# Kernel tuning notes

Measured on AMD Instinct MI355X. Metric: run time of the kernel, lower is better.

The kernel has to match this reference:

```python
import jax, jax.numpy as jnp
import numpy as np

N, DIM, K = 65536, 256, 4096

def setup_inputs() -> dict:
    key = jax.random.key(0)
    kx, kc = jax.random.split(key)
    x = jax.random.normal(kx, (N, DIM), dtype=jnp.float32)
    codebook = jax.random.normal(kc, (K, DIM), dtype=jnp.float32) * 0.02
    return {"x": x, "codebook": codebook}

def reference(x, codebook):
    # torch.cdist(x, codebook).argmin(-1) == argmin of squared distances;
    x_sq = jnp.sum(x * x, axis=-1, keepdims=True)           # (n, 1)
    c_sq = jnp.sum(codebook * codebook, axis=-1)            # (k,)
    dots = jnp.einsum('nd,kd->nk', x, codebook)             # (n, k) GEMM
    dist_sq = x_sq - 2.0 * dots + c_sq[None, :]             # (n, k)
    indices = jnp.argmin(dist_sq, axis=-1)                  # (n,)
    quantized = jnp.take(codebook, indices, axis=0)         # (n, dim) gather
    return (quantized, indices)
```

## Files before the change

### kernel.cpp

```cpp
#include <hip/hip_runtime.h>
#include <cfloat>

typedef _Float16 half8 __attribute__((ext_vector_type(8)));
typedef float    f32x4 __attribute__((ext_vector_type(4)));

#define N_ROWS 65536
#define DIM    256
#define KCODES 4096
#define BM 128
#define BN 128
#define BK 32
#define NSLICE (DIM / BK)
#define NCHUNK (KCODES / BN)

#define WS_CSQ 0
#define WS_CH  278528
#define WS_CL  2375680

#define GLDS(g, l) __builtin_amdgcn_global_load_lds(                       \
    (const __attribute__((address_space(1))) unsigned int*)(g),            \
    (__attribute__((address_space(3))) unsigned int*)(l), 16, 0, 0)

__global__ void prep_codes(const float* __restrict__ cb, float* __restrict__ csq,
                           _Float16* __restrict__ ch, _Float16* __restrict__ cl) {
    __shared__ float As[32 * DIM];
    const int t = threadIdx.x;
    const int c0 = blockIdx.x * 32;
    #pragma unroll
    for (int i = 0; i < 8; ++i) {
        int r = 4 * i + (t >> 6), d4 = (t & 63) * 4;
        *(float4*)&As[r * DIM + d4] = *(const float4*)&cb[(size_t)(c0 + r) * DIM + d4];
    }
    __syncthreads();
    {
        const int r = t >> 3;
        const int k0 = (t & 7) * 32;
        const float* src = &As[r * DIM + k0];
        _Float16* dh = &ch[(size_t)(c0 + r) * DIM + k0];
        _Float16* dl = &cl[(size_t)(c0 + r) * DIM + k0];
        #pragma unroll
        for (int i = 0; i < 4; ++i) {
            half8 hv, lv;
            #pragma unroll
            for (int j = 0; j < 8; ++j) {
                float sv = src[i * 8 + j] * 64.f;
                _Float16 h = (_Float16)sv;
                hv[j] = h; lv[j] = (_Float16)(sv - (float)h);
            }
            *(half8*)(dh + i * 8) = hv;
            *(half8*)(dl + i * 8) = lv;
        }
    }
    if (t < 32) {
        const float* row = &As[t * DIM];
        float s = 0.f;
        for (int k = 0; k < DIM; ++k) s = fmaf(row[k], row[k], s);
        csq[c0 + t] = s;
    }
}

__global__ __launch_bounds__(256, 2)
void vq_mfma(const float* __restrict__ x, const float* __restrict__ cb,
             const float* __restrict__ csq,
             const _Float16* __restrict__ ch, const _Float16* __restrict__ cl,
             float* out_q, float* __restrict__ out_idx) {
    __shared__ _Float16 LDS[8 * BM * BK];
    _Float16* AhS = LDS;
    _Float16* AlS = LDS + 2 * BM * BK;
    _Float16* BhS = LDS + 4 * BM * BK;
    _Float16* BlS = LDS + 6 * BM * BK;

    const int t = threadIdx.x;
    const int lane = t & 63, wave = t >> 6;
    const int wy = wave >> 1, wx = wave & 1;
    const int m = lane & 15, q = lane >> 4;
    const int n0 = blockIdx.x * BM;
    const int swz = (q ^ ((m + (m >> 2)) & 3)) * 8;

    {
        float*  prepF = (float*)LDS;
        double* dtmp  = (double*)(LDS + 4 * BM * BK);
        float*  xsqS  = (float*)(LDS + 6 * BM * BK);
        char*   xqw   = (char*)out_q;
        for (int g = 0; g < 4; ++g) {
            const int r0 = g * 32;
            #pragma unroll
            for (int i = 0; i < 8; ++i) {
                int r = 4 * i + (t >> 6), d4 = (t & 63) * 4;
                *(float4*)&prepF[r * DIM + d4] =
                    *(const float4*)&x[(size_t)(n0 + r0 + r) * DIM + d4];
            }
            __syncthreads();
            {
                const int r = t >> 3;
                const int col8 = (t & 7) * 8;
                char* dst = xqw + (((size_t)(n0 + r0 + r)) << 10) + (size_t)(col8 * 2);
                const float* src = &prepF[r * DIM + col8];
                #pragma unroll
                for (int i = 0; i < 4; ++i) {
                    half8 hv, lv;
                    #pragma unroll
                    for (int j = 0; j < 8; ++j) {
                        float v = src[i * 64 + j];
                        _Float16 h = (_Float16)v;
                        hv[j] = h; lv[j] = (_Float16)(v - (float)h);
                    }
                    *(half8*)(dst + i * 128) = hv;
                    *(half8*)(dst + 512 + i * 128) = lv;
                }
            }
            if (t < 128) {
                int r = t >> 2, part = t & 3;
                const float* ap = &prepF[r * DIM + 64 * part];
                double s = 0.0;
                for (int k = 0; k < 64; ++k) { double v = (double)ap[k]; s = fma(v, v, s); }
                dtmp[t] = s;
            }
            __syncthreads();
            if (t < 32)
                xsqS[r0 + t] = (float)((dtmp[4*t] + dtmp[4*t+1]) + (dtmp[4*t+2] + dtmp[4*t+3]));
            __syncthreads();
        }
    }

    float xsq_r[16];
    {
        const float* xsqS = (const float*)(LDS + 6 * BM * BK);
        #pragma unroll
        for (int s = 0; s < 16; ++s)
            xsq_r[s] = xsqS[64 * wy + 16 * (s >> 2) + 4 * q + (s & 3)];
    }
    asm volatile("s_waitcnt vmcnt(0)" ::: "memory");
    __syncthreads();

    const int rq  = lane >> 2;
    const int gph = lane & 3;
    const int glogB = ((gph ^ ((rq + (rq >> 2)) & 3)) << 4);
    const char* xqb = (const char*)out_q;
    const char* aBase  = xqb + (((size_t)(n0 + wave * 32 + rq)) << 10) + glogB;
    const char* bBaseH = (const char*)ch + (((size_t)(wave * 32 + rq)) << 9) + glogB;
    const char* bBaseL = (const char*)cl + (((size_t)(wave * 32 + rq)) << 9) + glogB;

#define STAGE(ck2, sl2, nb) do {                                             \
    const char* a_  = aBase  + (size_t)((sl2) * 64);                         \
    const size_t bo_ = ((size_t)(ck2) << 16) + (size_t)((sl2) * 64);         \
    const char* bh_ = bBaseH + bo_;                                          \
    const char* bl_ = bBaseL + bo_;                                          \
    _Float16* Ah_ = AhS + (nb) * (BM * BK) + wave * (32 * BK);               \
    _Float16* Al_ = AlS + (nb) * (BM * BK) + wave * (32 * BK);               \
    _Float16* Bh_ = BhS + (nb) * (BN * BK) + wave * (32 * BK);               \
    _Float16* Bl_ = BlS + (nb) * (BN * BK) + wave * (32 * BK);               \
    GLDS(a_,           Ah_);                                                 \
    GLDS(a_ + 16384,   Ah_ + 16 * BK);                                       \
    GLDS(a_ + 512,     Al_);                                                 \
    GLDS(a_ + 16896,   Al_ + 16 * BK);                                       \
    GLDS(bh_,          Bh_);                                                 \
    GLDS(bh_ + 8192,   Bh_ + 16 * BK);                                       \
    GLDS(bl_,          Bl_);                                                 \
    GLDS(bl_ + 8192,   Bl_ + 16 * BK);                                       \
} while (0)

    int aoffs[4], boffs[4];
    #pragma unroll
    for (int tr = 0; tr < 4; ++tr) aoffs[tr] = (64 * wy + 16 * tr + m) * BK + swz;
    #pragma unroll
    for (int tc = 0; tc < 4; ++tc) boffs[tc] = (64 * wx + 16 * tc + m) * BK + swz;

    float best[16]; int bidx[16];
    #pragma unroll
    for (int s = 0; s < 16; ++s) { best[s] = FLT_MAX; bidx[s] = 0; }

    STAGE(0, 0, 0);
    STAGE(0, 1, 1);
    asm volatile("s_waitcnt vmcnt(8)" ::: "memory");
    __builtin_amdgcn_s_barrier();
    __builtin_amdgcn_sched_barrier(0);

    for (int chunk = 0; chunk < NCHUNK; ++chunk) {
        const int c0 = chunk * BN;
        float csq_c[4];
        #pragma unroll
        for (int tc = 0; tc < 4; ++tc) csq_c[tc] = csq[c0 + 64 * wx + 16 * tc + m];

        f32x4 acc[4][4];
        #pragma unroll
        for (int tr = 0; tr < 4; ++tr)
            #pragma unroll
            for (int tc = 0; tc < 4; ++tc) acc[tr][tc] = (f32x4){0.f, 0.f, 0.f, 0.f};

        #pragma unroll
        for (int sl = 0; sl < NSLICE; ++sl) {
            const int cbuf = sl & 1;
            const _Float16* Ahr = AhS + cbuf * (BM * BK);
            const _Float16* Alr = AlS + cbuf * (BM * BK);
            const _Float16* Bhr = BhS + cbuf * (BN * BK);
            const _Float16* Blr = BlS + cbuf * (BN * BK);

            half8 aH[4], aL[4], bH[4], bL[4];
            #pragma unroll
            for (int tr = 0; tr < 4; ++tr) {
                aH[tr] = *(const half8*)&Ahr[aoffs[tr]];
                aL[tr] = *(const half8*)&Alr[aoffs[tr]];
            }
            #pragma unroll
            for (int tc = 0; tc < 4; ++tc) {
                bH[tc] = *(const half8*)&Bhr[boffs[tc]];
                bL[tc] = *(const half8*)&Blr[boffs[tc]];
            }

            const int sl2r = sl + 2;
            const int ck2 = chunk + (sl2r >> 3);
            const int sl2 = sl2r & 7;
            const bool stg = (ck2 < NCHUNK);
            if (stg) {
                asm volatile("s_waitcnt lgkmcnt(0)" ::: "memory");
                __builtin_amdgcn_s_barrier();
                __builtin_amdgcn_sched_barrier(0);
                STAGE(ck2, sl2, cbuf);
            }

            #pragma unroll
            for (int tc = 0; tc < 4; ++tc)
                #pragma unroll
                for (int tr = 0; tr < 4; ++tr)
                    acc[tr][tc] = __builtin_amdgcn_mfma_f32_16x16x32_f16(aH[tr], bH[tc], acc[tr][tc], 0, 0, 0);
            #pragma unroll
            for (int tc = 0; tc < 4; ++tc)
                #pragma unroll
                for (int tr = 0; tr < 4; ++tr)
                    acc[tr][tc] = __builtin_amdgcn_mfma_f32_16x16x32_f16(aH[tr], bL[tc], acc[tr][tc], 0, 0, 0);
            #pragma unroll
            for (int tc = 0; tc < 4; ++tc)
                #pragma unroll
                for (int tr = 0; tr < 4; ++tr)
                    acc[tr][tc] = __builtin_amdgcn_mfma_f32_16x16x32_f16(aL[tr], bH[tc], acc[tr][tc], 0, 0, 0);

            if (sl == NSLICE - 1) {
                #pragma unroll
                for (int tc = 0; tc < 4; ++tc) {
                    int c = c0 + 64 * wx + 16 * tc + m;
                    #pragma unroll
                    for (int tr = 0; tr < 4; ++tr) {
                        #pragma unroll
                        for (int e = 0; e < 4; ++e) {
                            float dot = acc[tr][tc][e] * 0.015625f;
                            float d = fmaf(-2.f, dot, xsq_r[tr * 4 + e]) + csq_c[tc];
                            int s = tr * 4 + e;
                            if (d < best[s]) { best[s] = d; bidx[s] = c; }
                        }
                    }
                }
            }

            if (!(chunk == NCHUNK - 1 && sl == NSLICE - 1)) {
                if (stg) asm volatile("s_waitcnt vmcnt(8)" ::: "memory");
                else     asm volatile("s_waitcnt vmcnt(0)" ::: "memory");
                __builtin_amdgcn_s_barrier();
                __builtin_amdgcn_sched_barrier(0);
            }
        }
    }

    #pragma unroll
    for (int s = 0; s < 16; ++s) {
        float v = best[s]; int idx = bidx[s];
        #pragma unroll
        for (int off = 1; off < 16; off <<= 1) {
            float v2 = __shfl_xor(v, off);
            int   i2 = __shfl_xor(idx, off);
            if (v2 < v || (v2 == v && i2 < idx)) { v = v2; idx = i2; }
        }
        best[s] = v; bidx[s] = idx;
    }
    __syncthreads();
    float* rb = (float*)BhS;
    int*   ri = (int*)BlS;
    {
        int s = m;
        int row_local = 64 * wy + 16 * (s >> 2) + 4 * q + (s & 3);
        rb[row_local * 2 + wx] = best[s];
        ri[row_local * 2 + wx] = bidx[s];
    }
    __syncthreads();
    int* widx = (int*)AhS;
    if (t < BM) {
        float d0 = rb[t * 2], d1 = rb[t * 2 + 1];
        int   i0 = ri[t * 2], i1 = ri[t * 2 + 1];
        int w = (d1 < d0 || (d1 == d0 && i1 < i0)) ? i1 : i0;
        widx[t] = w;
        out_idx[n0 + t] = (float)w;
    }
    __syncthreads();
    const int l4 = t & 63, rg = t >> 6;
    #pragma unroll 4
    for (int i = 0; i < 32; ++i) {
        int r = rg + 4 * i;
        *(float4*)&out_q[(size_t)(n0 + r) * DIM + l4 * 4] =
            *(const float4*)&cb[(size_t)widx[r] * DIM + l4 * 4];
    }
#undef STAGE
}

extern "C" void kernel_launch(void* const* d_in, const int* in_sizes, int n_in,
                              void* d_out, int out_size, void* d_ws, size_t ws_size,
                              hipStream_t stream) {
    const float* x  = (const float*)d_in[0];
    const float* cb = (const float*)d_in[1];
    float* out_q   = (float*)d_out;
    float* out_idx = (float*)d_out + (size_t)N_ROWS * DIM;

    float*    csq = (float*)((char*)d_ws + WS_CSQ);
    _Float16* ch  = (_Float16*)((char*)d_ws + WS_CH);
    _Float16* cl  = (_Float16*)((char*)d_ws + WS_CL);

    prep_codes<<<KCODES / 32, 256, 0, stream>>>(cb, csq, ch, cl);
    vq_mfma<<<N_ROWS / BM, 256, 0, stream>>>(x, cb, csq, ch, cl, out_q, out_idx);
}
```

Before: 578.5 us.

## Widen codebook tile to 256 codes per pass, reusing A fragments across two halves

The GEMM loop is restructured so each iteration covers 256 codes split into two 128-code accumulator sets, with the A fragments loaded from LDS once and reused for both. The A tile becomes single-buffered and is restaged every slice, while B stays double-buffered at twice the size. The x-norm values move from registers to a global workspace and are reloaded at each epilogue to free registers for the second accumulator set. LDS rises to 80 KB and register pressure doubles, which may cut occupancy below the launch-bounds target of two blocks. Each iteration now waits for all outstanding loads (vmcnt(0)) before the barrier, which reduces overlap between loads and compute.

```diff
diff --git a/kernel.cpp b/kernel.cpp
--- a/kernel.cpp
+++ b/kernel.cpp
@@ -8,12 +8,11 @@
 #define DIM    256
 #define KCODES 4096
 #define BM 128
-#define BN 128
 #define BK 32
-#define NSLICE (DIM / BK)
-#define NCHUNK (KCODES / BN)
+#define NITER 128
 
 #define WS_CSQ 0
+#define WS_XSQ 16384
 #define WS_CH  278528
 #define WS_CL  2375680
 
@@ -63,12 +62,12 @@
 void vq_mfma(const float* __restrict__ x, const float* __restrict__ cb,
              const float* __restrict__ csq,
              const _Float16* __restrict__ ch, const _Float16* __restrict__ cl,
-             float* out_q, float* __restrict__ out_idx) {
-    __shared__ _Float16 LDS[8 * BM * BK];
-    _Float16* AhS = LDS;
-    _Float16* AlS = LDS + 2 * BM * BK;
-    _Float16* BhS = LDS + 4 * BM * BK;
-    _Float16* BlS = LDS + 6 * BM * BK;
+             float* __restrict__ xsqg, float* out_q, float* __restrict__ out_idx) {
+    __shared__ __align__(1024) char SMEM[81920];
+    _Float16* AhS = (_Float16*)SMEM;
+    _Float16* AlS = (_Float16*)(SMEM + 8192);
+    _Float16* BhS = (_Float16*)(SMEM + 16384);
+    _Float16* BlS = (_Float16*)(SMEM + 49152);
 
     const int t = threadIdx.x;
     const int lane = t & 63, wave = t >> 6;
@@ -78,9 +77,8 @@
     const int swz = (q ^ ((m + (m >> 2)) & 3)) * 8;
 
     {
-        float*  prepF = (float*)LDS;
-        double* dtmp  = (double*)(LDS + 4 * BM * BK);
-        float*  xsqS  = (float*)(LDS + 6 * BM * BK);
+        float*  prepF = (float*)SMEM;
+        double* dtmp  = (double*)(SMEM + 49152);
         char*   xqw   = (char*)out_q;
         for (int g = 0; g < 4; ++g) {
             const int r0 = g * 32;
@@ -118,146 +116,166 @@
             }
             __syncthreads();
             if (t < 32)
-                xsqS[r0 + t] = (float)((dtmp[4*t] + dtmp[4*t+1]) + (dtmp[4*t+2] + dtmp[4*t+3]));
+                xsqg[n0 + r0 + t] = (float)((dtmp[4*t] + dtmp[4*t+1]) + (dtmp[4*t+2] + dtmp[4*t+3]));
             __syncthreads();
         }
-    }
-
-    float xsq_r[16];
-    {
-        const float* xsqS = (const float*)(LDS + 6 * BM * BK);
-        #pragma unroll
-        for (int s = 0; s < 16; ++s)
-            xsq_r[s] = xsqS[64 * wy + 16 * (s >> 2) + 4 * q + (s & 3)];
     }
     asm volatile("s_waitcnt vmcnt(0)" ::: "memory");
     __syncthreads();
 
     const int rq  = lane >> 2;
     const int gph = lane & 3;
-    const int glogB = ((gph ^ ((rq + (rq >> 2)) & 3)) << 4);
-    const char* xqb = (const char*)out_q;
-    const char* aBase  = xqb + (((size_t)(n0 + wave * 32 + rq)) << 10) + glogB;
-    const char* bBaseH = (const char*)ch + (((size_t)(wave * 32 + rq)) << 9) + glogB;
-    const char* bBaseL = (const char*)cl + (((size_t)(wave * 32 + rq)) << 9) + glogB;
-
-#define STAGE(ck2, sl2, nb) do {                                             \
-    const char* a_  = aBase  + (size_t)((sl2) * 64);                         \
-    const size_t bo_ = ((size_t)(ck2) << 16) + (size_t)((sl2) * 64);         \
+    const int glog = ((gph ^ ((rq + (rq >> 2)) & 3)) << 4);
+    const char* aBase  = (const char*)out_q + (((size_t)(n0 + wave * 32 + rq)) << 10) + glog;
+    const char* bBaseH = (const char*)ch + (((size_t)(wave * 64 + rq)) << 9) + glog;
+    const char* bBaseL = (const char*)cl + (((size_t)(wave * 64 + rq)) << 9) + glog;
+
+#define ASTAGE(s) do {                                                       \
+    const char* a_ = aBase + (size_t)((s) * 64);                             \
+    _Float16* Ah_ = AhS + wave * 1024;                                       \
+    _Float16* Al_ = AlS + wave * 1024;                                       \
+    GLDS(a_,           Ah_);                                                 \
+    GLDS(a_ + 16384,   Ah_ + 512);                                           \
+    GLDS(a_ + 512,     Al_);                                                 \
+    GLDS(a_ + 16896,   Al_ + 512);                                           \
+} while (0)
+
+#define BSTAGE(p2, s, nb) do {                                               \
+    const size_t bo_ = (size_t)(p2) * 131072 + (size_t)((s) * 64);           \
     const char* bh_ = bBaseH + bo_;                                          \
     const char* bl_ = bBaseL + bo_;                                          \
-    _Float16* Ah_ = AhS + (nb) * (BM * BK) + wave * (32 * BK);               \
-    _Float16* Al_ = AlS + (nb) * (BM * BK) + wave * (32 * BK);               \
-    _Float16* Bh_ = BhS + (nb) * (BN * BK) + wave * (32 * BK);               \
-    _Float16* Bl_ = BlS + (nb) * (BN * BK) + wave * (32 * BK);               \
-    GLDS(a_,           Ah_);                                                 \
-    GLDS(a_ + 16384,   Ah_ + 16 * BK);                                       \
-    GLDS(a_ + 512,     Al_);                                                 \
-    GLDS(a_ + 16896,   Al_ + 16 * BK);                                       \
+    _Float16* Bh_ = BhS + (nb) * 8192 + wave * 2048;                         \
+    _Float16* Bl_ = BlS + (nb) * 8192 + wave * 2048;                         \
     GLDS(bh_,          Bh_);                                                 \
-    GLDS(bh_ + 8192,   Bh_ + 16 * BK);                                       \
+    GLDS(bh_ + 8192,   Bh_ + 512);                                           \
+    GLDS(bh_ + 16384,  Bh_ + 1024);                                          \
+    GLDS(bh_ + 24576,  Bh_ + 1536);                                          \
     GLDS(bl_,          Bl_);                                                 \
-    GLDS(bl_ + 8192,   Bl_ + 16 * BK);                                       \
+    GLDS(bl_ + 8192,   Bl_ + 512);                                           \
+    GLDS(bl_ + 16384,  Bl_ + 1024);                                          \
+    GLDS(bl_ + 24576,  Bl_ + 1536);                                          \
 } while (0)
 
-    int aoffs[4], boffs[4];
-    #pragma unroll
-    for (int tr = 0; tr < 4; ++tr) aoffs[tr] = (64 * wy + 16 * tr + m) * BK + swz;
-    #pragma unroll
-    for (int tc = 0; tc < 4; ++tc) boffs[tc] = (64 * wx + 16 * tc + m) * BK + swz;
+#define SWEEP(AF, BF, ACC)                                                   \
+    _Pragma("unroll")                                                        \
+    for (int tc = 0; tc < 4; ++tc)                                           \
+        _Pragma("unroll")                                                    \
+        for (int tr = 0; tr < 4; ++tr)                                       \
+            ACC[tr][tc] = __builtin_amdgcn_mfma_f32_16x16x32_f16(AF[tr], BF[tc], ACC[tr][tc], 0, 0, 0)
+
+    const int a_rd = (64 * wy + m) * 32 + swz;
+    const int b_rd = (64 * wx + m) * 32 + swz;
 
     float best[16]; int bidx[16];
     #pragma unroll
     for (int s = 0; s < 16; ++s) { best[s] = FLT_MAX; bidx[s] = 0; }
 
-    STAGE(0, 0, 0);
-    STAGE(0, 1, 1);
-    asm volatile("s_waitcnt vmcnt(8)" ::: "memory");
+    ASTAGE(0);
+    BSTAGE(0, 0, 0);
+    BSTAGE(0, 1, 1);
+    asm volatile("s_waitcnt vmcnt(0)" ::: "memory");
     __builtin_amdgcn_s_barrier();
     __builtin_amdgcn_sched_barrier(0);
 
-    for (int chunk = 0; chunk < NCHUNK; ++chunk) {
-        const int c0 = chunk * BN;
-        float csq_c[4];
-        #pragma unroll
-        for (int tc = 0; tc < 4; ++tc) csq_c[tc] = csq[c0 + 64 * wx + 16 * tc + m];
-
-        f32x4 acc[4][4];
-        #pragma unroll
-        for (int tr = 0; tr < 4; ++tr)
+    f32x4 acc0[4][4], acc1[4][4];
+
+    #pragma unroll 2
+    for (int j = 0; j < NITER; ++j) {
+        const int cbuf = j & 1;
+        const int p2 = j >> 3, sl = j & 7;
+        if (sl == 0) {
             #pragma unroll
-            for (int tc = 0; tc < 4; ++tc) acc[tr][tc] = (f32x4){0.f, 0.f, 0.f, 0.f};
-
-        #pragma unroll
-        for (int sl = 0; sl < NSLICE; ++sl) {
-            const int cbuf = sl & 1;
-            const _Float16* Ahr = AhS + cbuf * (BM * BK);
-            const _Float16* Alr = AlS + cbuf * (BM * BK);
-            const _Float16* Bhr = BhS + cbuf * (BN * BK);
-            const _Float16* Blr = BlS + cbuf * (BN * BK);
-
-            half8 aH[4], aL[4], bH[4], bL[4];
+            for (int tr = 0; tr < 4; ++tr)
+                #pragma unroll
+                for (int tc = 0; tc < 4; ++tc) {
+                    acc0[tr][tc] = (f32x4){0.f, 0.f, 0.f, 0.f};
+                    acc1[tr][tc] = (f32x4){0.f, 0.f, 0.f, 0.f};
+                }
+        }
+        const _Float16* Bh = BhS + cbuf * 8192;
+        const _Float16* Bl = BlS + cbuf * 8192;
+
+        half8 aH[4], aL[4], b0h[4], b0l[4];
+        #pragma unroll
+        for (int tr = 0; tr < 4; ++tr) aH[tr] = *(const half8*)&AhS[a_rd + tr * 512];
+        #pragma unroll
+        for (int tc = 0; tc < 4; ++tc) b0h[tc] = *(const half8*)&Bh[b_rd + tc * 512];
+        #pragma unroll
+        for (int tc = 0; tc < 4; ++tc) b0l[tc] = *(const half8*)&Bl[b_rd + tc * 512];
+        #pragma unroll
+        for (int tr = 0; tr < 4; ++tr) aL[tr] = *(const half8*)&AlS[a_rd + tr * 512];
+
+        SWEEP(aH, b0h, acc0);
+        SWEEP(aH, b0l, acc0);
+        SWEEP(aL, b0h, acc0);
+
+        __builtin_amdgcn_sched_barrier(0x0F);
+        half8 b1h[4], b1l[4];
+        #pragma unroll
+        for (int tc = 0; tc < 4; ++tc) b1h[tc] = *(const half8*)&Bh[b_rd + 4096 + tc * 512];
+        #pragma unroll
+        for (int tc = 0; tc < 4; ++tc) b1l[tc] = *(const half8*)&Bl[b_rd + 4096 + tc * 512];
+
+        asm volatile("s_waitcnt lgkmcnt(0)" ::: "memory");
+        __builtin_amdgcn_s_barrier();
+        __builtin_amdgcn_sched_barrier(0);
+        if (j <= NITER - 2) ASTAGE((j + 1) & 7);
+        if (j <= NITER - 3) { const int jn = j + 2; BSTAGE(jn >> 3, jn & 7, cbuf); }
+        __builtin_amdgcn_sched_barrier(0);
+
+        SWEEP(aH, b1h, acc1);
+        SWEEP(aH, b1l, acc1);
+        SWEEP(aL, b1h, acc1);
+
+        if (sl == 7) {
+            float xr[16];
             #pragma unroll
-            for (int tr = 0; tr < 4; ++tr) {
-                aH[tr] = *(const half8*)&Ahr[aoffs[tr]];
-                aL[tr] = *(const half8*)&Alr[aoffs[tr]];
-            }
-            #pragma unroll
-            for (int tc = 0; tc < 4; ++tc) {
-                bH[tc] = *(const half8*)&Bhr[boffs[tc]];
-                bL[tc] = *(const half8*)&Blr[boffs[tc]];
-            }
-
-            const int sl2r = sl + 2;
-            const int ck2 = chunk + (sl2r >> 3);
-            const int sl2 = sl2r & 7;
-            const bool stg = (ck2 < NCHUNK);
-            if (stg) {
-                asm volatile("s_waitcnt lgkmcnt(0)" ::: "memory");
-                __builtin_amdgcn_s_barrier();
-                __builtin_amdgcn_sched_barrier(0);
-                STAGE(ck2, sl2, cbuf);
-            }
-
-            #pragma unroll
-            for (int tc = 0; tc < 4; ++tc)
-                #pragma unroll
-                for (int tr = 0; tr < 4; ++tr)
-                    acc[tr][tc] = __builtin_amdgcn_mfma_f32_16x16x32_f16(aH[tr], bH[tc], acc[tr][tc], 0, 0, 0);
-            #pragma unroll
-            for (int tc = 0; tc < 4; ++tc)
-                #pragma unroll
-                for (int tr = 0; tr < 4; ++tr)
-                    acc[tr][tc] = __builtin_amdgcn_mfma_f32_16x16x32_f16(aH[tr], bL[tc], acc[tr][tc], 0, 0, 0);
-            #pragma unroll
-            for (int tc = 0; tc < 4; ++tc)
-                #pragma unroll
-                for (int tr = 0; tr < 4; ++tr)
-                    acc[tr][tc] = __builtin_amdgcn_mfma_f32_16x16x32_f16(aL[tr], bH[tc], acc[tr][tc], 0, 0, 0);
-
-            if (sl == NSLICE - 1) {
+            for (int s = 0; s < 16; ++s)
+                xr[s] = xsqg[n0 + 64 * wy + 16 * (s >> 2) + 4 * q + (s & 3)];
+            {
+                const int cb0 = 256 * p2 + 64 * wx;
+                float cs[4];
+                #pragma unroll
+                for (int tc = 0; tc < 4; ++tc) cs[tc] = csq[cb0 + 16 * tc + m];
                 #pragma unroll
                 for (int tc = 0; tc < 4; ++tc) {
-                    int c = c0 + 64 * wx + 16 * tc + m;
+                    int c = cb0 + 16 * tc + m;
                     #pragma unroll
-                    for (int tr = 0; tr < 4; ++tr) {
+                    for (int tr = 0; tr < 4; ++tr)
                         #pragma unroll
                         for (int e = 0; e < 4; ++e) {
-                            float dot = acc[tr][tc][e] * 0.015625f;
-                            float d = fmaf(-2.f, dot, xsq_r[tr * 4 + e]) + csq_c[tc];
+                            float dot = acc0[tr][tc][e] * 0.015625f;
+                            float d = fmaf(-2.f, dot, xr[tr * 4 + e]) + cs[tc];
                             int s = tr * 4 + e;
                             if (d < best[s]) { best[s] = d; bidx[s] = c; }
                         }
-                    }
                 }
             }
-
-            if (!(chunk == NCHUNK - 1 && sl == NSLICE - 1)) {
-                if (stg) asm volatile("s_waitcnt vmcnt(8)" ::: "memory");
-                else     asm volatile("s_waitcnt vmcnt(0)" ::: "memory");
-                __builtin_amdgcn_s_barrier();
-                __builtin_amdgcn_sched_barrier(0);
-            }
+            {
+                const int cb1 = 256 * p2 + 128 + 64 * wx;
+                float cs[4];
+                #pragma unroll
+                for (int tc = 0; tc < 4; ++tc) cs[tc] = csq[cb1 + 16 * tc + m];
+                #pragma unroll
+                for (int tc = 0; tc < 4; ++tc) {
+                    int c = cb1 + 16 * tc + m;
+                    #pragma unroll
+                    for (int tr = 0; tr < 4; ++tr)
+                        #pragma unroll
+                        for (int e = 0; e < 4; ++e) {
+                            float dot = acc1[tr][tc][e] * 0.015625f;
+                            float d = fmaf(-2.f, dot, xr[tr * 4 + e]) + cs[tc];
+                            int s = tr * 4 + e;
+                            if (d < best[s]) { best[s] = d; bidx[s] = c; }
+                        }
+                }
+            }
+        }
+
+        if (j < NITER - 1) {
+            asm volatile("s_waitcnt vmcnt(0)" ::: "memory");
+            __builtin_amdgcn_s_barrier();
+            __builtin_amdgcn_sched_barrier(0);
         }
     }
 
@@ -273,8 +291,8 @@
         best[s] = v; bidx[s] = idx;
     }
     __syncthreads();
-    float* rb = (float*)BhS;
-    int*   ri = (int*)BlS;
+    float* rb = (float*)SMEM;
+    int*   ri = (int*)(SMEM + 16384);
     {
         int s = m;
         int row_local = 64 * wy + 16 * (s >> 2) + 4 * q + (s & 3);
@@ -282,7 +300,7 @@
         ri[row_local * 2 + wx] = bidx[s];
     }
     __syncthreads();
-    int* widx = (int*)AhS;
+    int* widx = (int*)(SMEM + 32768);
     if (t < BM) {
         float d0 = rb[t * 2], d1 = rb[t * 2 + 1];
         int   i0 = ri[t * 2], i1 = ri[t * 2 + 1];
@@ -298,7 +316,9 @@
         *(float4*)&out_q[(size_t)(n0 + r) * DIM + l4 * 4] =
             *(const float4*)&cb[(size_t)widx[r] * DIM + l4 * 4];
     }
-#undef STAGE
+#undef ASTAGE
+#undef BSTAGE
+#undef SWEEP
 }
 
 extern "C" void kernel_launch(void* const* d_in, const int* in_sizes, int n_in,
@@ -309,10 +329,11 @@
     float* out_q   = (float*)d_out;
     float* out_idx = (float*)d_out + (size_t)N_ROWS * DIM;
 
-    float*    csq = (float*)((char*)d_ws + WS_CSQ);
-    _Float16* ch  = (_Float16*)((char*)d_ws + WS_CH);
-    _Float16* cl  = (_Float16*)((char*)d_ws + WS_CL);
+    float*    csq  = (float*)((char*)d_ws + WS_CSQ);
+    float*    xsqg = (float*)((char*)d_ws + WS_XSQ);
+    _Float16* ch   = (_Float16*)((char*)d_ws + WS_CH);
+    _Float16* cl   = (_Float16*)((char*)d_ws + WS_CL);
 
     prep_codes<<<KCODES / 32, 256, 0, stream>>>(cb, csq, ch, cl);
-    vq_mfma<<<N_ROWS / BM, 256, 0, stream>>>(x, cb, csq, ch, cl, out_q, out_idx);
+    vq_mfma<<<N_ROWS / BM, 256, 0, stream>>>(x, cb, csq, ch, cl, xsqg, out_q, out_idx);
 }
```

After: 777.6 us. 1.34x slower.
